# Optimization experiments

Hardware: AMD Instinct MI355X
Metric: run time of the kernel (lower is better)

Reference implementation:

```python
import jax, jax.numpy as jnp
import numpy as np

NUM_HEADS = 8
GROUP = 16
LN_EPS = 1e-5

def _star_relu(x, scale, bias):
    return scale * jnp.square(jax.nn.relu(x)) + bias

def _layernorm(x, w, b):
    mu = x.mean(-1, keepdims=True)
    var = jnp.mean(jnp.square(x - mu), -1, keepdims=True)
    return (x - mu) / jnp.sqrt(var + LN_EPS) * w + b

def _attention(x, qkv_w, proj_w, proj_b, pa_scale, pa_bias, lf_w, lf_b, hf_w, hf_b, lf_gamma, hf_gamma):
    B, N, C = x.shape
    hd = C // NUM_HEADS
    detail = _star_relu(x, pa_scale, pa_bias)
    lf = jnp.tanh(detail @ lf_w.T + lf_b)                      # (B,N,H)
    hf = jax.nn.softplus(detail @ hf_w.T + hf_b)
    hf_sq = jnp.square(hf)
    hf = 2.0 * hf_sq / (hf_sq + 0.3678)
    lf = jnp.repeat(lf, hd, axis=-1)                           # (B,N,C): per-head value repeated across head_dim
    hf = jnp.repeat(hf, hd, axis=-1)
    qkv = (x @ qkv_w.T).reshape(B, N, 3, NUM_HEADS, hd).transpose(2, 0, 3, 1, 4)
    q, k, v = qkv[0], qkv[1], qkv[2]
    q = q * (hd ** -0.5)
    attn = jax.nn.softmax(jnp.einsum('bhqd,bhkd->bhqk', q, k), axis=-1)
    attn_out = jnp.einsum('bhqk,bhkd->bhqd', attn, v).transpose(0, 2, 1, 3).reshape(B, N, C)
    value_tokens = v.transpose(0, 2, 1, 3).reshape(B, N, C)
    high_res = value_tokens - attn_out
    attn_out = attn_out + attn_out * lf * lf_gamma + hf * high_res * hf_gamma
    return attn_out @ proj_w.T + proj_b

def _freq_scale(x, rw1_w, rw1_scale, rw1_bias, rw2_w, freq_w):
    # x: (B,C,H,W); freq_w: (num_filters, C//group, base_size, base_size//2+1) == rfft grid
    B, C, H, W = x.shape
    xf = jnp.fft.rfft2(x, axes=(2, 3), norm='ortho')           # (B,C,fh,fw) complex
    pooled = x.mean(axis=(2, 3))                               # (B,C)
    h = _star_relu(pooled @ rw1_w.T, rw1_scale, rw1_bias)
    routing = jnp.tanh((h @ rw2_w.T).reshape(B, GROUP, -1))    # (B,g,f)
    fh, fw = xf.shape[2], xf.shape[3]
    dyn = jnp.einsum('bgf,fchw->bgchw', routing, freq_w).reshape(B, C, fh, fw)
    xf = xf * dyn
    return jnp.fft.irfft2(xf, s=(H, W), axes=(2, 3), norm='ortho')

def _forward(x, norm1_w, norm1_b, qkv_w, proj_w, proj_b, pa_scale, pa_bias, lf_w, lf_b, hf_w, hf_b,
             lf_gamma, hf_gamma, fs1_rw1_w, fs1_rw1_scale, fs1_rw1_bias, fs1_rw2_w, fs1_fw, gamma_1,
             norm2_w, norm2_b, fc1_w, fc1_b, fc2_w, fc2_b, fs2_rw1_w, fs2_rw1_scale, fs2_rw1_bias,
             fs2_rw2_w, fs2_fw, gamma_2):
    B, C, H, W = x.shape
    tokens = x.reshape(B, C, H * W).transpose(0, 2, 1)         # nchw -> nlc
    att_tokens = _attention(_layernorm(tokens, norm1_w, norm1_b),
                            qkv_w, proj_w, proj_b, pa_scale, pa_bias,
                            lf_w, lf_b, hf_w, hf_b, lf_gamma, hf_gamma)
    att_feat = att_tokens.transpose(0, 2, 1).reshape(B, C, H, W)
    att_feat = _freq_scale(att_feat, fs1_rw1_w, fs1_rw1_scale, fs1_rw1_bias, fs1_rw2_w, fs1_fw) + att_feat
    att_tokens = att_feat.reshape(B, C, H * W).transpose(0, 2, 1)
    tokens = tokens + gamma_1 * att_tokens
    h = _layernorm(tokens, norm2_w, norm2_b)
    mlp_tokens = jax.nn.gelu(h @ fc1_w.T + fc1_b, approximate=False) @ fc2_w.T + fc2_b
    mlp_feat = mlp_tokens.transpose(0, 2, 1).reshape(B, C, H, W)
    mlp_feat = _freq_scale(mlp_feat, fs2_rw1_w, fs2_rw1_scale, fs2_rw1_bias, fs2_rw2_w, fs2_fw) + mlp_feat
    mlp_tokens = mlp_feat.reshape(B, C, H * W).transpose(0, 2, 1)
    tokens = tokens + gamma_2 * mlp_tokens
    return tokens.transpose(0, 2, 1).reshape(B, C, H, W)

def setup_inputs() -> dict:
    key = jax.random.key(0)
    ks = jax.random.split(key, 16)
    B, C, H, W = 16, 512, 32, 32
    heads, group, nf, bs = 8, 16, 4, 32
    hid_rw = int(C * 0.125)
    hid_mlp = int(C * 4.0)
    bfs = bs // 2 + 1
    d = {}
    d['x'] = jax.random.normal(ks[0], (B, C, H, W), jnp.float32)
    d['norm1_w'] = jnp.ones((C,), jnp.float32); d['norm1_b'] = jnp.zeros((C,), jnp.float32)
    d['qkv_w'] = jax.random.normal(ks[1], (3 * C, C), jnp.float32) * 0.02
    d['proj_w'] = jax.random.normal(ks[2], (C, C), jnp.float32) * 0.02
    d['proj_b'] = jnp.zeros((C,), jnp.float32)
    d['pa_scale'] = jnp.ones((1,), jnp.float32); d['pa_bias'] = jnp.zeros((1,), jnp.float32)
    d['lf_w'] = jax.random.normal(ks[3], (heads, C), jnp.float32) * 0.02
    d['lf_b'] = jnp.zeros((heads,), jnp.float32)
    d['hf_w'] = jax.random.normal(ks[4], (heads, C), jnp.float32) * 0.02
    d['hf_b'] = jnp.zeros((heads,), jnp.float32)
    d['lf_gamma'] = 1e-5 * jnp.ones((C,), jnp.float32)
    d['hf_gamma'] = 1e-5 * jnp.ones((C,), jnp.float32)
    d['fs1_rw1_w'] = jax.random.normal(ks[5], (hid_rw, C), jnp.float32) * 0.02
    d['fs1_rw1_scale'] = jnp.ones((1,), jnp.float32); d['fs1_rw1_bias'] = jnp.zeros((1,), jnp.float32)
    d['fs1_rw2_w'] = jax.random.normal(ks[6], (group * nf, hid_rw), jnp.float32) * 0.02
    d['fs1_fw'] = jax.random.normal(ks[7], (nf, C // group, bs, bfs), jnp.float32) * 1e-5
    d['gamma_1'] = 1e-4 * jnp.ones((C,), jnp.float32)
    d['norm2_w'] = jnp.ones((C,), jnp.float32); d['norm2_b'] = jnp.zeros((C,), jnp.float32)
    d['fc1_w'] = jax.random.normal(ks[8], (hid_mlp, C), jnp.float32) * 0.02
    d['fc1_b'] = jnp.zeros((hid_mlp,), jnp.float32)
    d['fc2_w'] = jax.random.normal(ks[9], (C, hid_mlp), jnp.float32) * 0.02
    d['fc2_b'] = jnp.zeros((C,), jnp.float32)
    d['fs2_rw1_w'] = jax.random.normal(ks[10], (hid_rw, C), jnp.float32) * 0.02
    d['fs2_rw1_scale'] = jnp.ones((1,), jnp.float32); d['fs2_rw1_bias'] = jnp.zeros((1,), jnp.float32)
    d['fs2_rw2_w'] = jax.random.normal(ks[11], (group * nf, hid_rw), jnp.float32) * 0.02
    d['fs2_fw'] = jax.random.normal(ks[12], (nf, C // group, bs, bfs), jnp.float32) * 1e-5
    d['gamma_2'] = 1e-4 * jnp.ones((C,), jnp.float32)
    return d

def reference(x, norm1_w, norm1_b, qkv_w, proj_w, proj_b, pa_scale, pa_bias, lf_w, lf_b, hf_w, hf_b,
              lf_gamma, hf_gamma, fs1_rw1_w, fs1_rw1_scale, fs1_rw1_bias, fs1_rw2_w, fs1_fw, gamma_1,
              norm2_w, norm2_b, fc1_w, fc1_b, fc2_w, fc2_b, fs2_rw1_w, fs2_rw1_scale, fs2_rw1_bias,
              fs2_rw2_w, fs2_fw, gamma_2):
    return _forward(x, norm1_w, norm1_b, qkv_w, proj_w, proj_b, pa_scale, pa_bias, lf_w, lf_b, hf_w, hf_b,
                    lf_gamma, hf_gamma, fs1_rw1_w, fs1_rw1_scale, fs1_rw1_bias, fs1_rw2_w, fs1_fw, gamma_1,
                    norm2_w, norm2_b, fc1_w, fc1_b, fc2_w, fc2_b, fs2_rw1_w, fs2_rw1_scale, fs2_rw1_bias,
                    fs2_rw2_w, fs2_fw, gamma_2)
```

## Files before the change

kernel.cpp:

```cpp
#include <hip/hip_runtime.h>
#include <cstdint>
#include <cstddef>

#define B_   16
#define C_   512
#define N_   1024
#define M_   (B_*N_)
#define NH_  8
#define HD_  64
#define C3_  1536
#define CH_  2048

typedef __attribute__((ext_vector_type(8))) short bf16x8;
typedef __attribute__((ext_vector_type(4))) float f32x4;
typedef __attribute__((ext_vector_type(4))) unsigned short u16x4;

__device__ __forceinline__ unsigned short f2bf(float f) {
  union { float f; unsigned u; } v; v.f = f;
  unsigned r = v.u + 0x7fffu + ((v.u >> 16) & 1u);
  return (unsigned short)(r >> 16);
}
__device__ __forceinline__ float bf2f(unsigned short h) {
  union { unsigned u; float f; } v; v.u = ((unsigned)h) << 16;
  return v.f;
}
__device__ __forceinline__ unsigned f2u(float f) {
  union { float f; unsigned u; } v; v.f = f; return v.u;
}

#define GL16(gp, lp) \
  __builtin_amdgcn_global_load_lds( \
      (const __attribute__((address_space(1))) unsigned int*)(const void*)(gp), \
      (__attribute__((address_space(3))) unsigned int*)(void*)(lp), 16, 0, 0)

__global__ __launch_bounds__(256) void k_f2b4(
    const float* __restrict__ s0, unsigned short* __restrict__ d0,
    const float* __restrict__ s1, unsigned short* __restrict__ d1,
    const float* __restrict__ s2, unsigned short* __restrict__ d2,
    const float* __restrict__ s3, unsigned short* __restrict__ d3) {
  int blk = blockIdx.x, t = threadIdx.x;
  const float* s; unsigned short* d; int off;
  if (blk < 3072)      { s = s0; d = d0; off = blk * 256; }
  else if (blk < 4096) { s = s1; d = d1; off = (blk - 3072) * 256; }
  else if (blk < 8192) { s = s2; d = d2; off = (blk - 4096) * 256; }
  else                 { s = s3; d = d3; off = (blk - 8192) * 256; }
  int i = off + t;
  d[i] = f2bf(s[i]);
}

__global__ __launch_bounds__(256) void k_twid(unsigned short* __restrict__ gtab,
                                              float* __restrict__ p1,
                                              float* __restrict__ p2) {
  int idx = blockIdx.x * 256 + threadIdx.x;
  if (idx < 6400) {
    int tab = idx / 1280, rem = idx % 1280;
    int i = rem / 40, j = rem % 40;
    float v = 0.f;
    if (j < 32) {
      float th = 0.19634954084936207f * (float)((i * j) & 31);
      float s, c;
      __sincosf(th, &s, &c);
      if (tab == 0) v = c;
      else if (tab == 1) v = s;
      else if (tab == 2) v = -s;
      else {
        float wg = (j == 0 || j == 16) ? 1.f : 2.f;
        if (j >= 17) wg = 0.f;
        v = (tab == 3) ? wg * c : -wg * s;
      }
    }
    gtab[idx] = f2bf(v);
  } else if (idx < 14592) {
    p1[idx - 6400] = 0.f;
  } else if (idx < 22784) {
    p2[idx - 14592] = 0.f;
  }
}

template<bool WITH>
__global__ __launch_bounds__(256) void k_lnt(const float* __restrict__ src,
    const float* __restrict__ w, const float* __restrict__ bia,
    const float* __restrict__ lfw, const float* __restrict__ lfb,
    const float* __restrict__ hfw, const float* __restrict__ hfb,
    const float* __restrict__ pa_s, const float* __restrict__ pa_b,
    unsigned short* __restrict__ lnout, float* __restrict__ lfout,
    float* __restrict__ hfout) {
  __shared__ unsigned short s[512 * 34];
  const int t = threadIdx.x, wv = t >> 6, l = t & 63;
  const int n0 = blockIdx.x * 32, b = blockIdx.y;
  const int cl = t >> 3;
  const int nn = (t & 7) * 4;
  #pragma unroll
  for (int k = 0; k < 16; ++k) {
    int c = k * 32 + cl;
    float4 v = *(const float4*)&src[(size_t)(b * C_ + c) * N_ + n0 + nn];
    s[c * 34 + nn]     = f2bf(v.x);
    s[c * 34 + nn + 1] = f2bf(v.y);
    s[c * 34 + nn + 2] = f2bf(v.z);
    s[c * 34 + nn + 3] = f2bf(v.w);
  }
  __syncthreads();
  float wv8[8], bv8[8];
  #pragma unroll
  for (int k = 0; k < 8; ++k) { wv8[k] = w[l + 64 * k]; bv8[k] = bia[l + 64 * k]; }
  float ps = 1.f, pb = 0.f;
  if (WITH) { ps = pa_s[0]; pb = pa_b[0]; }
  for (int ri = 0; ri < 8; ++ri) {
    const int n = wv * 8 + ri;
    const int row = b * N_ + n0 + n;
    float v[8];
    #pragma unroll
    for (int k = 0; k < 8; ++k) v[k] = bf2f(s[(l + 64 * k) * 34 + n]);
    float sm = 0.f, q = 0.f;
    #pragma unroll
    for (int k = 0; k < 8; ++k) { sm += v[k]; q += v[k] * v[k]; }
    #pragma unroll
    for (int off = 1; off < 64; off <<= 1) { sm += __shfl_xor(sm, off); q += __shfl_xor(q, off); }
    float mu = sm * (1.f / 512.f);
    float var = q * (1.f / 512.f) - mu * mu;
    float rstd = rsqrtf(var + 1e-5f);
    float ln[8];
    #pragma unroll
    for (int k = 0; k < 8; ++k) ln[k] = (v[k] - mu) * rstd * wv8[k] + bv8[k];
    #pragma unroll
    for (int k = 0; k < 8; ++k)
      lnout[(size_t)row * C_ + l + 64 * k] = f2bf(ln[k]);
    if (WITH) {
      float d[8];
      #pragma unroll
      for (int k = 0; k < 8; ++k) { float r = fmaxf(ln[k], 0.f); d[k] = ps * r * r + pb; }
      float lacc[8], hacc[8];
      #pragma unroll
      for (int h = 0; h < 8; ++h) {
        float la = 0.f, ha = 0.f;
        #pragma unroll
        for (int k = 0; k < 8; ++k) {
          la += d[k] * lfw[h * C_ + l + 64 * k];
          ha += d[k] * hfw[h * C_ + l + 64 * k];
        }
        lacc[h] = la; hacc[h] = ha;
      }
      #pragma unroll
      for (int h = 0; h < 8; ++h)
        #pragma unroll
        for (int off = 1; off < 64; off <<= 1) {
          lacc[h] += __shfl_xor(lacc[h], off);
          hacc[h] += __shfl_xor(hacc[h], off);
        }
      float lv = lacc[0], hv = hacc[0];
      #pragma unroll
      for (int h = 1; h < 8; ++h) { if (l == h) { lv = lacc[h]; hv = hacc[h]; } }
      if (l < 8) {
        lfout[(size_t)row * 8 + l] = tanhf(lv + lfb[l]);
        float z = hv + hfb[l];
        float sp = (z > 15.f) ? z : log1pf(__expf(z));
        float s2 = sp * sp;
        hfout[(size_t)row * 8 + l] = 2.f * s2 / (s2 + 0.3678f);
      }
    }
  }
}

template<int EPI>
__global__ __launch_bounds__(256) void k_gemm(const unsigned short* __restrict__ A,
    const unsigned short* __restrict__ Bt, const float* __restrict__ bias,
    void* __restrict__ outv, unsigned short* __restrict__ vtg, int Nn, int K, int nx) {
  __shared__ __align__(16) unsigned short Asm[2 * 128 * 32];
  __shared__ __align__(16) unsigned short Bsm[2 * 128 * 32];
  const int t = threadIdx.x, w = t >> 6, l = t & 63;
  const int lane15 = l & 15, quad = l >> 4;
  const int cpx = gridDim.x >> 3;
  const int wgs = (blockIdx.x & 7) * cpx + (blockIdx.x >> 3);
  const int bx = wgs % nx, by = wgs / nx;
  const int n0 = bx * 128, m0 = by * 128;
  const int wm = w >> 1, wn = w & 1;
  f32x4 acc[4][4];
  #pragma unroll
  for (int i = 0; i < 4; ++i)
    #pragma unroll
    for (int j = 0; j < 4; ++j) acc[i][j] = (f32x4){0.f, 0.f, 0.f, 0.f};
  const int srow = w * 16 + (l >> 2);
  const int scol = (l & 3) * 8;
  const unsigned short* gA = A + (size_t)(m0 + srow) * K + scol;
  const unsigned short* gB = Bt + (size_t)(n0 + srow) * K + scol;
  const size_t rk64 = (size_t)64 * K;
  auto stage = [&](int bufi, int k0) {
    char* a = (char*)Asm + bufi * 8192 + w * 1024;
    char* bb = (char*)Bsm + bufi * 8192 + w * 1024;
    GL16(gA + k0, a);
    GL16(gA + k0 + rk64, a + 4096);
    GL16(gB + k0, bb);
    GL16(gB + k0 + rk64, bb + 4096);
  };
  stage(0, 0);
  __syncthreads();
  for (int k0 = 0; k0 < K; k0 += 32) {
    const int cur = (k0 >> 5) & 1;
    if (k0 + 32 < K) stage(cur ^ 1, k0 + 32);
    const unsigned short* As = Asm + cur * 4096;
    const unsigned short* Bs = Bsm + cur * 4096;
    bf16x8 af[4], bg[4];
    #pragma unroll
    for (int i = 0; i < 4; ++i)
      af[i] = *(const bf16x8*)&As[(wm * 64 + i * 16 + lane15) * 32 + quad * 8];
    #pragma unroll
    for (int i = 0; i < 4; ++i)
      bg[i] = *(const bf16x8*)&Bs[(wn * 64 + i * 16 + lane15) * 32 + quad * 8];
    #pragma unroll
    for (int i = 0; i < 4; ++i)
      #pragma unroll
      for (int j = 0; j < 4; ++j)
        acc[i][j] = __builtin_amdgcn_mfma_f32_16x16x32_bf16(af[i], bg[j], acc[i][j], 0, 0, 0);
    __syncthreads();
  }
  float psum[4] = {0.f, 0.f, 0.f, 0.f};
  #pragma unroll
  for (int i = 0; i < 4; ++i) {
    int grow = m0 + wm * 64 + i * 16 + quad * 4;
    int bq = grow >> 10, nq = grow & 1023;
    #pragma unroll
    for (int j = 0; j < 4; ++j) {
      int gcol = n0 + wn * 64 + j * 16 + lane15;
      float bs = (EPI == 0) ? 0.f : bias[gcol];
      if (EPI == 1 || EPI == 3) {
        float4 o = make_float4(acc[i][j][0] + bs, acc[i][j][1] + bs,
                               acc[i][j][2] + bs, acc[i][j][3] + bs);
        psum[j] += o.x + o.y + o.z + o.w;
        u16x4 pv = { f2bf(o.x), f2bf(o.y), f2bf(o.z), f2bf(o.w) };
        *(u16x4*)&((unsigned short*)outv)[((size_t)(bq * C_ + gcol) << 10) + nq] = pv;
      } else if (EPI == 0) {
        u16x4 pv;
        #pragma unroll
        for (int r = 0; r < 4; ++r) {
          unsigned short hv = f2bf(acc[i][j][r]);
          pv[r] = hv;
          ((unsigned short*)outv)[(size_t)(grow + r) * Nn + gcol] = hv;
        }
        if (gcol >= 1024)
          *(u16x4*)&vtg[((size_t)(bq * C_ + gcol - 1024) << 10) + nq] = pv;
      } else {
        #pragma unroll
        for (int r = 0; r < 4; ++r) {
          float vv = acc[i][j][r] + bs;
          float e = __builtin_amdgcn_exp2f(-(2.302118073f * vv +
                                             0.1029455568f * vv * vv * vv));
          float g = vv * __builtin_amdgcn_rcpf(1.f + e);
          ((unsigned short*)outv)[(size_t)(grow + r) * Nn + gcol] = f2bf(g);
        }
      }
    }
  }
  if (EPI == 1 || EPI == 3) {
    float* pooled = (float*)vtg;
    const int bq = m0 >> 10;
    #pragma unroll
    for (int j = 0; j < 4; ++j) {
      float v = psum[j] * (1.f / 1024.f);
      v += __shfl_xor(v, 16);
      v += __shfl_xor(v, 32);
      if (quad == 0) {
        int gcol = n0 + wn * 64 + j * 16 + lane15;
        atomicAdd(&pooled[bq * C_ + gcol], v);
      }
    }
  }
}

__global__ __launch_bounds__(256, 4) void k_flash(const unsigned short* __restrict__ qkv,
    const unsigned short* __restrict__ vtg, const float* __restrict__ lf,
    const float* __restrict__ hf, const float* __restrict__ lgam,
    const float* __restrict__ hgam, unsigned short* __restrict__ y) {
  const int t = threadIdx.x, w = t >> 6, l = t & 63;
  const int lane15 = l & 15, quad = l >> 4;
  const int wg = (blockIdx.x & 7) * 128 + (blockIdx.x >> 3);
  const int qt = wg & 7;
  const int h = (wg >> 3) & 7;
  const int b = wg >> 6;
  const int q0 = qt * 128;

  __shared__ __align__(16) unsigned short kt[64 * 64];
  __shared__ __align__(16) unsigned short vt[64 * 64];
  __shared__ __align__(16) unsigned short pl[4][16 * 72];

  bf16x8 aq[2][2];
  #pragma unroll
  for (int qh = 0; qh < 2; ++qh) {
    const unsigned short* qp = qkv +
        (size_t)(b * N_ + q0 + w * 32 + qh * 16 + lane15) * C3_ + h * 64 + quad * 8;
    bf16x8 r0 = *(const bf16x8*)qp;
    bf16x8 r1 = *(const bf16x8*)(qp + 32);
    #pragma unroll
    for (int i = 0; i < 8; ++i) {
      aq[qh][0][i] = (short)f2bf(0.1803368801111713f * bf2f((unsigned short)r0[i]));
      aq[qh][1][i] = (short)f2bf(0.1803368801111713f * bf2f((unsigned short)r1[i]));
    }
  }
  f32x4 O[2][4];
  #pragma unroll
  for (int qh = 0; qh < 2; ++qh)
    #pragma unroll
    for (int i = 0; i < 4; ++i) O[qh][i] = (f32x4){0.f, 0.f, 0.f, 0.f};
  float lsum[2] = {0.f, 0.f};

  const int prow = w * 8 + (l >> 3);
  const int csw = ((l & 7) ^ (l >> 3)) * 8;
  const unsigned short* kg = qkv + (size_t)(b * N_ + prow) * C3_ + 512 + h * 64 + csw;
  const unsigned short* vg = vtg + (size_t)((b * NH_ + h) * HD_ + prow) * N_ + csw;
  char* ktb0 = (char*)kt + w * 1024;
  char* ktb1 = (char*)kt + 4096 + w * 1024;
  char* vtb0 = (char*)vt + w * 1024;
  char* vtb1 = (char*)vt + 4096 + w * 1024;
  const int swx = (lane15 & 7) * 8;

  for (int kti = 0; kti < 16; ++kti) {
    __syncthreads();
    const unsigned short* kr = kg + (size_t)(kti * 64) * C3_;
    GL16(kr, ktb0);
    GL16(kr + (size_t)32 * C3_, ktb1);
    const unsigned short* vr = vg + kti * 64;
    GL16(vr, vtb0);
    GL16(vr + 32 * N_, vtb1);
    __syncthreads();

    #pragma unroll
    for (int qh = 0; qh < 2; ++qh) {
      f32x4 S[4];
      __builtin_amdgcn_s_setprio(1);
      #pragma unroll
      for (int nt = 0; nt < 4; ++nt) {
        const int nrow = nt * 16 + lane15;
        bf16x8 ak0 = *(const bf16x8*)&kt[nrow * 64 + ((quad * 8) ^ swx)];
        bf16x8 ak1 = *(const bf16x8*)&kt[nrow * 64 + ((32 + quad * 8) ^ swx)];
        f32x4 z = (f32x4){0.f, 0.f, 0.f, 0.f};
        z = __builtin_amdgcn_mfma_f32_16x16x32_bf16(ak0, aq[qh][0], z, 0, 0, 0);
        z = __builtin_amdgcn_mfma_f32_16x16x32_bf16(ak1, aq[qh][1], z, 0, 0, 0);
        S[nt] = z;
      }
      __builtin_amdgcn_s_setprio(0);
      #pragma unroll
      for (int nt = 0; nt < 4; ++nt)
        #pragma unroll
        for (int r = 0; r < 4; ++r) {
          float pv = __builtin_amdgcn_exp2f(S[nt][r]);
          S[nt][r] = pv;
          lsum[qh] += pv;
        }
      #pragma unroll
      for (int nt = 0; nt < 4; ++nt) {
        unsigned lo = __builtin_amdgcn_perm(f2u(S[nt][1]), f2u(S[nt][0]), 0x07060302u);
        unsigned hi = __builtin_amdgcn_perm(f2u(S[nt][3]), f2u(S[nt][2]), 0x07060302u);
        *(uint2*)&pl[w][lane15 * 72 + nt * 16 + quad * 4] = make_uint2(lo, hi);
      }
      __builtin_amdgcn_s_setprio(1);
      #pragma unroll
      for (int nc = 0; nc < 2; ++nc) {
        bf16x8 ap = *(const bf16x8*)&pl[w][lane15 * 72 + nc * 32 + quad * 8];
        #pragma unroll
        for (int dt = 0; dt < 4; ++dt) {
          const int vrow = dt * 16 + lane15;
          bf16x8 bv = *(const bf16x8*)&vt[vrow * 64 + ((nc * 32 + quad * 8) ^ swx)];
          O[qh][dt] = __builtin_amdgcn_mfma_f32_16x16x32_bf16(ap, bv, O[qh][dt], 0, 0, 0);
        }
      }
      __builtin_amdgcn_s_setprio(0);
    }
  }

  #pragma unroll
  for (int qh = 0; qh < 2; ++qh) {
    float s = lsum[qh];
    s += __shfl_xor(s, 16);
    s += __shfl_xor(s, 32);
    float inv = 1.f / s;
    float invr[4], lfr[4], hfr[4];
    const size_t rowb = (size_t)(b * N_ + q0 + w * 32 + qh * 16 + quad * 4);
    #pragma unroll
    for (int r = 0; r < 4; ++r) {
      invr[r] = __shfl(inv, quad * 4 + r);
      lfr[r] = lf[(rowb + r) * 8 + h];
      hfr[r] = hf[(rowb + r) * 8 + h];
    }
    #pragma unroll
    for (int dt = 0; dt < 4; ++dt) {
      const int cc = h * 64 + dt * 16 + lane15;
      const float lg = lgam[cc], hg = hgam[cc];
      #pragma unroll
      for (int r = 0; r < 4; ++r) {
        float a = O[qh][dt][r] * invr[r];
        float vval = bf2f(qkv[(rowb + r) * C3_ + 1024 + cc]);
        float res = a + a * lfr[r] * lg + hfr[r] * (vval - a) * hg;
        y[(rowb + r) * C_ + cc] = f2bf(res);
      }
    }
  }
}

__global__ __launch_bounds__(256) void k_routing(const float* __restrict__ pooled,
    const float* __restrict__ rw1, const float* __restrict__ rw1s,
    const float* __restrict__ rw1b, const float* __restrict__ rw2,
    float* __restrict__ routing) {
  const int b = blockIdx.x, t = threadIdx.x;
  __shared__ float plds[512];
  __shared__ float tile[64][65];
  __shared__ float hl[64];
  plds[t] = pooled[b * 512 + t];
  plds[t + 256] = pooled[b * 512 + t + 256];
  __syncthreads();
  float acc = 0.f;
  for (int c0 = 0; c0 < 512; c0 += 64) {
    #pragma unroll
    for (int kk = 0; kk < 16; ++kk) {
      int idx = kk * 256 + t;
      tile[idx >> 6][idx & 63] = rw1[(size_t)(idx >> 6) * 512 + c0 + (idx & 63)];
    }
    __syncthreads();
    if (t < 64) {
      #pragma unroll
      for (int i = 0; i < 64; ++i) acc += plds[c0 + i] * tile[t][i];
    }
    __syncthreads();
  }
  if (t < 64) {
    float r = fmaxf(acc, 0.f);
    hl[t] = rw1s[0] * r * r + rw1b[0];
  }
  __syncthreads();
  if (t < 64) {
    float r2 = 0.f;
    #pragma unroll
    for (int j = 0; j < 64; ++j) r2 += hl[j] * rw2[(size_t)t * 64 + j];
    routing[b * 64 + t] = tanhf(r2);
  }
}

__global__ __launch_bounds__(256) void k_freq(const unsigned short* __restrict__ feat,
    const float* __restrict__ routing, const float* __restrict__ fwtab,
    const unsigned short* __restrict__ gtab, const float* __restrict__ res,
    const float* __restrict__ gamma, float* __restrict__ outp) {
  const int c = blockIdx.x, b = blockIdx.y, t = threadIdx.x;
  const int g = c >> 5, cc = c & 31;
  const int w = t >> 6, l = t & 63;
  const int lane15 = l & 15, quad = l >> 4;
  const int mt = w & 1, nt = w >> 1;
  __shared__ __align__(16) unsigned short Xbf[32 * 40];
  __shared__ __align__(16) float p[32 * 36];
  __shared__ __align__(16) unsigned short Tabs[6400];
  __shared__ __align__(16) unsigned short pl1r[32 * 40], pl1i[32 * 40];
  __shared__ __align__(16) unsigned short pl2r[32 * 40], pl2i[32 * 40];
  __shared__ __align__(16) unsigned short pl3r[32 * 40], pl3i[32 * 40];
  __shared__ float Ms[1024];
  const size_t base = (size_t)(b * C_ + c) * N_;

  {
    u16x4 xb = *(const u16x4*)&feat[base + t * 4];
    float4 v = make_float4(bf2f(xb[0]), bf2f(xb[1]), bf2f(xb[2]), bf2f(xb[3]));
    int hh = t >> 3, w4 = (t & 7) * 4;
    *(float4*)&p[hh * 36 + w4] = v;
    *(u16x4*)&Xbf[hh * 40 + w4] = xb;
  }
  {
    const uint4* src = (const uint4*)gtab;
    uint4* dst = (uint4*)Tabs;
    #pragma unroll
    for (int k = 0; k < 4; ++k) {
      int o = k * 256 + t;
      if (o < 800) dst[o] = src[o];
    }
  }
  {
    float r0 = routing[b * 64 + g * 4 + 0];
    float r1 = routing[b * 64 + g * 4 + 1];
    float r2 = routing[b * 64 + g * 4 + 2];
    float r3 = routing[b * 64 + g * 4 + 3];
    const float* fb = fwtab + (size_t)cc * 544;
    #pragma unroll
    for (int k = 0; k < 4; ++k) {
      int o = k * 256 + t;
      int fh = o >> 5, fw = o & 31;
      float mv = 0.f;
      if (fw < 17) {
        int fi = fh * 17 + fw;
        mv = (r0 * fb[fi] + r1 * fb[17408 + fi] + r2 * fb[34816 + fi] +
              r3 * fb[52224 + fi]) * (1.f / 1024.f);
      }
      Ms[o] = mv;
    }
  }
  __syncthreads();

  const unsigned short* Tc  = Tabs;
  const unsigned short* Ts  = Tabs + 1280;
  const unsigned short* Tsn = Tabs + 2560;
  const unsigned short* Tcw = Tabs + 3840;
  const unsigned short* Tsw = Tabs + 5120;
  const int arow = (mt * 16 + lane15) * 40 + quad * 8;
  const int brow = (nt * 16 + lane15) * 40 + quad * 8;
  const int prow = (nt * 16 + lane15) * 40 + mt * 16 + quad * 4;
  const f32x4 zz = (f32x4){0.f, 0.f, 0.f, 0.f};

  {
    bf16x8 aX = *(const bf16x8*)&Xbf[arow];
    bf16x8 bC = *(const bf16x8*)&Tc[brow];
    bf16x8 bS = *(const bf16x8*)&Tsn[brow];
    f32x4 re = __builtin_amdgcn_mfma_f32_16x16x32_bf16(aX, bC, zz, 0, 0, 0);
    f32x4 im = __builtin_amdgcn_mfma_f32_16x16x32_bf16(aX, bS, zz, 0, 0, 0);
    uint2 pr = make_uint2(__builtin_amdgcn_perm(f2u(re[1]), f2u(re[0]), 0x07060302u),
                          __builtin_amdgcn_perm(f2u(re[3]), f2u(re[2]), 0x07060302u));
    uint2 pi = make_uint2(__builtin_amdgcn_perm(f2u(im[1]), f2u(im[0]), 0x07060302u),
                          __builtin_amdgcn_perm(f2u(im[3]), f2u(im[2]), 0x07060302u));
    *(uint2*)&pl1r[prow] = pr;
    *(uint2*)&pl1i[prow] = pi;
  }
  __syncthreads();
  {
    bf16x8 aC = *(const bf16x8*)&Tc[arow];
    bf16x8 aS = *(const bf16x8*)&Ts[arow];
    bf16x8 aN = *(const bf16x8*)&Tsn[arow];
    bf16x8 bR = *(const bf16x8*)&pl1r[brow];
    bf16x8 bI = *(const bf16x8*)&pl1i[brow];
    f32x4 er = __builtin_amdgcn_mfma_f32_16x16x32_bf16(aC, bR, zz, 0, 0, 0);
    er = __builtin_amdgcn_mfma_f32_16x16x32_bf16(aS, bI, er, 0, 0, 0);
    f32x4 ei = __builtin_amdgcn_mfma_f32_16x16x32_bf16(aC, bI, zz, 0, 0, 0);
    ei = __builtin_amdgcn_mfma_f32_16x16x32_bf16(aN, bR, ei, 0, 0, 0);
    #pragma unroll
    for (int r = 0; r < 4; ++r) {
      float mk = Ms[(mt * 16 + quad * 4 + r) * 32 + nt * 16 + lane15];
      er[r] *= mk; ei[r] *= mk;
    }
    uint2 pr = make_uint2(__builtin_amdgcn_perm(f2u(er[1]), f2u(er[0]), 0x07060302u),
                          __builtin_amdgcn_perm(f2u(er[3]), f2u(er[2]), 0x07060302u));
    uint2 pi = make_uint2(__builtin_amdgcn_perm(f2u(ei[1]), f2u(ei[0]), 0x07060302u),
                          __builtin_amdgcn_perm(f2u(ei[3]), f2u(ei[2]), 0x07060302u));
    *(uint2*)&pl2r[prow] = pr;
    *(uint2*)&pl2i[prow] = pi;
  }
  __syncthreads();
  {
    bf16x8 aR = *(const bf16x8*)&pl2r[arow];
    bf16x8 aI = *(const bf16x8*)&pl2i[arow];
    bf16x8 bC = *(const bf16x8*)&Tc[brow];
    bf16x8 bS = *(const bf16x8*)&Ts[brow];
    bf16x8 bN = *(const bf16x8*)&Tsn[brow];
    f32x4 zr = __builtin_amdgcn_mfma_f32_16x16x32_bf16(aR, bC, zz, 0, 0, 0);
    zr = __builtin_amdgcn_mfma_f32_16x16x32_bf16(aI, bN, zr, 0, 0, 0);
    f32x4 zi = __builtin_amdgcn_mfma_f32_16x16x32_bf16(aI, bC, zz, 0, 0, 0);
    zi = __builtin_amdgcn_mfma_f32_16x16x32_bf16(aR, bS, zi, 0, 0, 0);
    uint2 pr = make_uint2(__builtin_amdgcn_perm(f2u(zr[1]), f2u(zr[0]), 0x07060302u),
                          __builtin_amdgcn_perm(f2u(zr[3]), f2u(zr[2]), 0x07060302u));
    uint2 pi = make_uint2(__builtin_amdgcn_perm(f2u(zi[1]), f2u(zi[0]), 0x07060302u),
                          __builtin_amdgcn_perm(f2u(zi[3]), f2u(zi[2]), 0x07060302u));
    *(uint2*)&pl3r[prow] = pr;
    *(uint2*)&pl3i[prow] = pi;
  }
  __syncthreads();
  {
    bf16x8 aC = *(const bf16x8*)&Tcw[arow];
    bf16x8 aS = *(const bf16x8*)&Tsw[arow];
    bf16x8 bR = *(const bf16x8*)&pl3r[brow];
    bf16x8 bI = *(const bf16x8*)&pl3i[brow];
    f32x4 y = __builtin_amdgcn_mfma_f32_16x16x32_bf16(aC, bR, zz, 0, 0, 0);
    y = __builtin_amdgcn_mfma_f32_16x16x32_bf16(aS, bI, y, 0, 0, 0);
    int hh = nt * 16 + lane15, w0 = mt * 16 + quad * 4;
    float4 fp = *(const float4*)&p[hh * 36 + w0];
    float4 rp = *(const float4*)&res[base + hh * 32 + w0];
    float gv = gamma[c];
    float4 o = make_float4(rp.x + gv * (y[0] + fp.x), rp.y + gv * (y[1] + fp.y),
                           rp.z + gv * (y[2] + fp.z), rp.w + gv * (y[3] + fp.w));
    *(float4*)&outp[base + hh * 32 + w0] = o;
  }
}

extern "C" void kernel_launch(void* const* d_in, const int* in_sizes, int n_in,
                              void* d_out, int out_size, void* d_ws, size_t ws_size,
                              hipStream_t stream) {
  (void)in_sizes; (void)n_in; (void)out_size; (void)ws_size;
  const float* x      = (const float*)d_in[0];
  const float* n1w    = (const float*)d_in[1];
  const float* n1b    = (const float*)d_in[2];
  const float* qkv_w  = (const float*)d_in[3];
  const float* proj_w = (const float*)d_in[4];
  const float* proj_b = (const float*)d_in[5];
  const float* pa_s   = (const float*)d_in[6];
  const float* pa_b   = (const float*)d_in[7];
  const float* lf_w   = (const float*)d_in[8];
  const float* lf_b   = (const float*)d_in[9];
  const float* hf_w   = (const float*)d_in[10];
  const float* hf_b   = (const float*)d_in[11];
  const float* lf_g   = (const float*)d_in[12];
  const float* hf_g   = (const float*)d_in[13];
  const float* f1rw1w = (const float*)d_in[14];
  const float* f1rw1s = (const float*)d_in[15];
  const float* f1rw1b = (const float*)d_in[16];
  const float* f1rw2w = (const float*)d_in[17];
  const float* f1fw   = (const float*)d_in[18];
  const float* gamma1 = (const float*)d_in[19];
  const float* n2w    = (const float*)d_in[20];
  const float* n2b    = (const float*)d_in[21];
  const float* fc1w   = (const float*)d_in[22];
  const float* fc1b   = (const float*)d_in[23];
  const float* fc2w   = (const float*)d_in[24];
  const float* fc2b   = (const float*)d_in[25];
  const float* f2rw1w = (const float*)d_in[26];
  const float* f2rw1s = (const float*)d_in[27];
  const float* f2rw1b = (const float*)d_in[28];
  const float* f2rw2w = (const float*)d_in[29];
  const float* f2fw   = (const float*)d_in[30];
  const float* gamma2 = (const float*)d_in[31];

  char* ws = (char*)d_ws;
  float*          tokens = (float*)(ws + 0);
  float*          f1buf  = (float*)(ws + 33554432ULL);
  unsigned short* featb  = (unsigned short*)(ws + 67108864ULL);
  unsigned short* regA   = (unsigned short*)(ws + 134217728ULL);
  unsigned short* abuf   = (unsigned short*)(ws + 201326592ULL);
  float*          lfbuf  = (float*)(ws + 218103808ULL);
  float*          hfbuf  = (float*)(ws + 218628096ULL);
  float*          pooled = (float*)(ws + 219152384ULL);
  float*          routing= (float*)(ws + 219185152ULL);
  unsigned short* wq     = (unsigned short*)(ws + 219189248ULL);
  unsigned short* wp     = (unsigned short*)(ws + 220762112ULL);
  unsigned short* w1     = (unsigned short*)(ws + 221286400ULL);
  unsigned short* w2     = (unsigned short*)(ws + 223383552ULL);
  unsigned short* gtab   = (unsigned short*)(ws + 225480704ULL);
  unsigned short* vtg    = (unsigned short*)f1buf;
  float*          pooled2= (float*)(ws + 50331648ULL);

  k_f2b4<<<12288, 256, 0, stream>>>(qkv_w, wq, proj_w, wp, fc1w, w1, fc2w, w2);
  k_twid<<<89, 256, 0, stream>>>(gtab, pooled, pooled2);

  k_lnt<true><<<dim3(32, 16), 256, 0, stream>>>(x, n1w, n1b, lf_w, lf_b, hf_w, hf_b,
                                                pa_s, pa_b, abuf, lfbuf, hfbuf);
  k_gemm<0><<<1536, 256, 0, stream>>>(abuf, wq, n1b, regA, vtg, C3_, C_, 12);
  k_flash<<<1024, 256, 0, stream>>>(regA, vtg, lfbuf, hfbuf, lf_g, hf_g, abuf);
  k_gemm<1><<<512, 256, 0, stream>>>(abuf, wp, proj_b, featb,
                                     (unsigned short*)pooled, C_, C_, 4);
  k_routing<<<16, 256, 0, stream>>>(pooled, f1rw1w, f1rw1s, f1rw1b, f1rw2w, routing);
  k_freq<<<dim3(512, 16), 256, 0, stream>>>(featb, routing, f1fw, gtab, x, gamma1, tokens);
  k_lnt<false><<<dim3(32, 16), 256, 0, stream>>>(tokens, n2w, n2b, nullptr, nullptr,
                                                 nullptr, nullptr, nullptr, nullptr,
                                                 abuf, nullptr, nullptr);
  k_gemm<2><<<2048, 256, 0, stream>>>(abuf, w1, fc1b, regA, nullptr, CH_, C_, 16);
  k_gemm<3><<<512, 256, 0, stream>>>(regA, w2, fc2b, featb,
                                     (unsigned short*)pooled2, C_, CH_, 4);
  k_routing<<<16, 256, 0, stream>>>(pooled2, f2rw1w, f2rw1s, f2rw1b, f2rw2w, routing);
  k_freq<<<dim3(512, 16), 256, 0, stream>>>(featb, routing, f2fw, gtab, tokens, gamma2,
                                            (float*)d_out);
}
```

Baseline: 487.3 us.

## Load K and V fragments directly from global memory in flash attention

Removes the shared-memory staging of K and V tiles and the two block-wide barriers per key tile in the flash kernel. Each wave now reads its K fragments into registers and its V fragments straight from global memory, relying on cache hits since all four waves read the same tiles. This frees LDS and barrier stalls but multiplies global/L2 traffic by four and exposes load latency inside the MFMA loop without prefetching, and V loads now sit inside the qh loop so they repeat.

```diff
diff --git a/kernel.cpp b/kernel.cpp
--- a/kernel.cpp
+++ b/kernel.cpp
@@ -278,8 +278,6 @@
   const int b = wg >> 6;
   const int q0 = qt * 128;
 
-  __shared__ __align__(16) unsigned short kt[64 * 64];
-  __shared__ __align__(16) unsigned short vt[64 * 64];
   __shared__ __align__(16) unsigned short pl[4][16 * 72];
 
   bf16x8 aq[2][2];
@@ -302,38 +300,26 @@
     for (int i = 0; i < 4; ++i) O[qh][i] = (f32x4){0.f, 0.f, 0.f, 0.f};
   float lsum[2] = {0.f, 0.f};
 
-  const int prow = w * 8 + (l >> 3);
-  const int csw = ((l & 7) ^ (l >> 3)) * 8;
-  const unsigned short* kg = qkv + (size_t)(b * N_ + prow) * C3_ + 512 + h * 64 + csw;
-  const unsigned short* vg = vtg + (size_t)((b * NH_ + h) * HD_ + prow) * N_ + csw;
-  char* ktb0 = (char*)kt + w * 1024;
-  char* ktb1 = (char*)kt + 4096 + w * 1024;
-  char* vtb0 = (char*)vt + w * 1024;
-  char* vtb1 = (char*)vt + 4096 + w * 1024;
-  const int swx = (lane15 & 7) * 8;
+  const unsigned short* kbase = qkv + (size_t)b * N_ * C3_ + 512 + h * 64 + quad * 8;
+  const unsigned short* vbase = vtg + (size_t)((b * NH_ + h) * HD_) * N_;
 
   for (int kti = 0; kti < 16; ++kti) {
-    __syncthreads();
-    const unsigned short* kr = kg + (size_t)(kti * 64) * C3_;
-    GL16(kr, ktb0);
-    GL16(kr + (size_t)32 * C3_, ktb1);
-    const unsigned short* vr = vg + kti * 64;
-    GL16(vr, vtb0);
-    GL16(vr + 32 * N_, vtb1);
-    __syncthreads();
-
+    bf16x8 kf[4][2];
+    #pragma unroll
+    for (int nt = 0; nt < 4; ++nt) {
+      const unsigned short* kp = kbase + (size_t)(kti * 64 + nt * 16 + lane15) * C3_;
+      kf[nt][0] = *(const bf16x8*)kp;
+      kf[nt][1] = *(const bf16x8*)(kp + 32);
+    }
     #pragma unroll
     for (int qh = 0; qh < 2; ++qh) {
       f32x4 S[4];
       __builtin_amdgcn_s_setprio(1);
       #pragma unroll
       for (int nt = 0; nt < 4; ++nt) {
-        const int nrow = nt * 16 + lane15;
-        bf16x8 ak0 = *(const bf16x8*)&kt[nrow * 64 + ((quad * 8) ^ swx)];
-        bf16x8 ak1 = *(const bf16x8*)&kt[nrow * 64 + ((32 + quad * 8) ^ swx)];
         f32x4 z = (f32x4){0.f, 0.f, 0.f, 0.f};
-        z = __builtin_amdgcn_mfma_f32_16x16x32_bf16(ak0, aq[qh][0], z, 0, 0, 0);
-        z = __builtin_amdgcn_mfma_f32_16x16x32_bf16(ak1, aq[qh][1], z, 0, 0, 0);
+        z = __builtin_amdgcn_mfma_f32_16x16x32_bf16(kf[nt][0], aq[qh][0], z, 0, 0, 0);
+        z = __builtin_amdgcn_mfma_f32_16x16x32_bf16(kf[nt][1], aq[qh][1], z, 0, 0, 0);
         S[nt] = z;
       }
       __builtin_amdgcn_s_setprio(0);
@@ -357,8 +343,8 @@
         bf16x8 ap = *(const bf16x8*)&pl[w][lane15 * 72 + nc * 32 + quad * 8];
         #pragma unroll
         for (int dt = 0; dt < 4; ++dt) {
-          const int vrow = dt * 16 + lane15;
-          bf16x8 bv = *(const bf16x8*)&vt[vrow * 64 + ((nc * 32 + quad * 8) ^ swx)];
+          bf16x8 bv = *(const bf16x8*)(vbase + (size_t)(dt * 16 + lane15) * N_ +
+                                       kti * 64 + nc * 32 + quad * 8);
           O[qh][dt] = __builtin_amdgcn_mfma_f32_16x16x32_bf16(ap, bv, O[qh][dt], 0, 0, 0);
         }
       }
```

Measured after the change: 564.6 us. 15.9% more time.
